# Performance work log

Hardware: AMD Instinct MI355X
Metric: run time of the kernel (lower is better)

Reference implementation:

```python
import jax, jax.numpy as jnp
import numpy as np


def setup_inputs() -> dict:
    key = jax.random.key(0)
    ks = jax.random.split(key, 8)
    B, T, D, H, R = 64, 1024, 512, 512, 64
    s = lambda n: 1.0 / np.sqrt(n)
    return {
        "x":   jax.random.normal(ks[0], (B, T, D), jnp.float32),
        "W_w": jax.random.normal(ks[1], (4 * H, D), jnp.float32) * s(D),
        "W_b": jax.random.normal(ks[2], (4 * H,), jnp.float32) * 0.01,
        "U_w": jax.random.normal(ks[3], (4 * H, H), jnp.float32) * s(H),
        "U_b": jax.random.normal(ks[4], (4 * H,), jnp.float32) * 0.01,
        "A_w": jax.random.normal(ks[5], (R, D), jnp.float32) * s(D),
        "B_w": jax.random.normal(ks[6], (R, H), jnp.float32) * s(H),
        "P_w": jax.random.normal(ks[7], (H, R), jnp.float32) * s(R),
    }


def reference(x, W_w, W_b, U_w, U_b, A_w, B_w, P_w):
    # x: [B,T,D]. Dropout is identity (eval mode).
    Bsz, T, _ = x.shape
    H = U_w.shape[0] // 4
    # Precompute all input-side projections in parallel (no recurrence dep).
    Wx = jnp.einsum('btd,hd->bth', x, W_w) + W_b          # [B,T,4H]
    Ax = jnp.einsum('btd,rd->btr', x, A_w)                # [B,T,R]

    def step(carry, inp):
        h, c = carry
        wx_t, ax_t = inp                                  # [B,4H], [B,R]
        gates = wx_t + h @ U_w.T + U_b                    # [B,4H]
        i, f, o, g = jnp.split(gates, 4, axis=-1)
        i = jax.nn.sigmoid(i)
        f = jax.nn.sigmoid(f)
        o = jax.nn.sigmoid(o)
        g = jnp.tanh(g)
        mix = (ax_t * (h @ B_w.T)) @ P_w.T                # [B,H]
        c = f * c + i * g + 0.1 * mix
        h = o * jnp.tanh(c)
        return (h, c), h

    h0 = jnp.zeros((Bsz, H), x.dtype)
    c0 = jnp.zeros((Bsz, H), x.dtype)
    (h, c), outs = jax.lax.scan(
        step, (h0, c0),
        (jnp.swapaxes(Wx, 0, 1), jnp.swapaxes(Ax, 0, 1)))
    outs = jnp.swapaxes(outs, 0, 1)                       # [B,T,H]
    return outs, h, c
```

## Files before the change

### kernel.cpp

```cpp
#include <hip/hip_runtime.h>
#include <stdint.h>


typedef float    f32x4  __attribute__((ext_vector_type(4)));
typedef __bf16   bf16x8 __attribute__((ext_vector_type(8)));
typedef uint16_t u16;
typedef uint16_t u16x8  __attribute__((ext_vector_type(8)));
typedef uint32_t u32x4  __attribute__((ext_vector_type(4)));

#define WS_XB     0
#define WS_WC     67108864
#define WS_BIAS   69337088
#define WS_U      69345792
#define WS_BW     71442944
#define WS_P      71508480
#define WS_HBUF   71574016
#define WS_MBOX   71705088
#define WS_WXC    71721472

#define OUT_H     33554432
#define OUT_C     33587200

__device__ __forceinline__ u16 f2bf(float f) {
  uint32_t u = __builtin_bit_cast(uint32_t, f);
  u = (u + 0x7fffu + ((u >> 16) & 1u)) >> 16;
  return (u16)u;
}
__device__ __forceinline__ float bf2f(u16 b) {
  uint32_t u = ((uint32_t)b) << 16;
  return __builtin_bit_cast(float, u);
}
__device__ __forceinline__ f32x4 mfma16(u16x8 a, u16x8 b, f32x4 c) {
  return __builtin_amdgcn_mfma_f32_16x16x32_bf16(
      __builtin_bit_cast(bf16x8, a), __builtin_bit_cast(bf16x8, b), c, 0, 0, 0);
}
__device__ __forceinline__ float sigm(float x) { return 1.f / (1.f + __expf(-x)); }
__device__ __forceinline__ float tanh_fast(float x) {
  float a = fabsf(x);
  float e = __expf(2.f * a);
  float t = 1.f - 2.f / (e + 1.f);
  return x < 0.f ? -t : t;
}
__device__ __forceinline__ void lds_barrier() {
  asm volatile("s_waitcnt lgkmcnt(0)" ::: "memory");
  __builtin_amdgcn_sched_barrier(0);
  __builtin_amdgcn_s_barrier();
  __builtin_amdgcn_sched_barrier(0);
}

__global__ void cast_x(const float* __restrict__ x, u16* __restrict__ xb) {
  int i = blockIdx.x * 256 + threadIdx.x;
  const float4* src = (const float4*)x;
  float4 a = src[(size_t)i * 2];
  float4 b = src[(size_t)i * 2 + 1];
  u16x8 o;
  o[0] = f2bf(a.x); o[1] = f2bf(a.y); o[2] = f2bf(a.z); o[3] = f2bf(a.w);
  o[4] = f2bf(b.x); o[5] = f2bf(b.y); o[6] = f2bf(b.z); o[7] = f2bf(b.w);
  *(u16x8*)(xb + (size_t)i * 8) = o;
}

__global__ void prep(const float* __restrict__ W_w, const float* __restrict__ W_b,
                     const float* __restrict__ U_w, const float* __restrict__ U_b,
                     const float* __restrict__ A_w, const float* __restrict__ B_w,
                     const float* __restrict__ P_w,
                     u16* __restrict__ Wc, float* __restrict__ bias,
                     u16* __restrict__ Ubf, u16* __restrict__ Bwbf,
                     u16* __restrict__ Pbf, uint32_t* __restrict__ mbox) {
  const int total = 1114112 + 1048576 + 32768 + 32768 + 2176 + 4096;
  for (int i = blockIdx.x * blockDim.x + threadIdx.x; i < total;
       i += gridDim.x * blockDim.x) {
    int idx = i;
    if (idx < 1114112) {
      int row = idx >> 9, k = idx & 511;
      float v = 0.f;
      if (row < 2048) v = W_w[row * 512 + k];
      else if (row < 2112) v = A_w[(row - 2048) * 512 + k];
      Wc[idx] = f2bf(v);
      continue;
    }
    idx -= 1114112;
    if (idx < 1048576) { Ubf[idx] = f2bf(U_w[idx]); continue; }
    idx -= 1048576;
    if (idx < 32768) { Bwbf[idx] = f2bf(B_w[idx]); continue; }
    idx -= 32768;
    if (idx < 32768) { Pbf[idx] = f2bf(0.1f * P_w[idx]); continue; }
    idx -= 32768;
    if (idx < 2176) {
      bias[idx] = (idx < 2048) ? (W_b[idx] + U_b[idx]) : 0.f;
      continue;
    }
    idx -= 2176;
    mbox[idx] = 0;
  }
}

__global__ void __launch_bounds__(256) gemm_wxc(const u16* __restrict__ xb,
                                                const u16* __restrict__ Wc,
                                                const float* __restrict__ bias,
                                                u16* __restrict__ outWx) {
  __shared__ u16 Atile[128 * 64];
  __shared__ u16 Btile[128 * 64];
  const int n0 = blockIdx.x * 128;
  const int m0 = blockIdx.y * 128;
  const int tid = threadIdx.x, ln = tid & 63, wv = tid >> 6;
  const int wm = (wv >> 1) * 64, wn = (wv & 1) * 64;
  f32x4 acc[4][4] = {};

  for (int k0 = 0; k0 < 512; k0 += 64) {
    __syncthreads();
    #pragma unroll
    for (int q = 0; q < 4; ++q) {
      int idx = tid + q * 256;
      int row = idx >> 3, kc = idx & 7;
      uint4 va = *(const uint4*)(xb + (size_t)(m0 + row) * 512 + k0 + kc * 8);
      *(uint4*)((char*)Atile + row * 128 + ((kc * 16) ^ ((row & 7) << 4))) = va;
      uint4 vb = *(const uint4*)(Wc + (size_t)(n0 + row) * 512 + k0 + kc * 8);
      *(uint4*)((char*)Btile + row * 128 + ((kc * 16) ^ ((row & 7) << 4))) = vb;
    }
    __syncthreads();
    #pragma unroll
    for (int kk = 0; kk < 64; kk += 32) {
      u16x8 af[4], bf[4];
      const int kb = kk * 2 + ((ln >> 4) << 4);
      #pragma unroll
      for (int i = 0; i < 4; ++i) {
        int arow = wm + i * 16 + (ln & 15);
        af[i] = *(const u16x8*)((char*)Atile + arow * 128 + (kb ^ ((arow & 7) << 4)));
        int brow = wn + i * 16 + (ln & 15);
        bf[i] = *(const u16x8*)((char*)Btile + brow * 128 + (kb ^ ((brow & 7) << 4)));
      }
      #pragma unroll
      for (int i = 0; i < 4; ++i)
        #pragma unroll
        for (int j = 0; j < 4; ++j)
          acc[i][j] = mfma16(af[i], bf[j], acc[i][j]);
    }
  }
  #pragma unroll
  for (int i = 0; i < 4; ++i) {
    const int mrow = m0 + wm + i * 16 + ((ln >> 4) << 2);
    #pragma unroll
    for (int j = 0; j < 4; ++j) {
      const int n = n0 + wn + j * 16 + (ln & 15);
      if (n < 2112) {
        const float bv = bias[n];
        #pragma unroll
        for (int r = 0; r < 4; ++r)
          outWx[(size_t)(mrow + r) * 2112 + n] = f2bf(acc[i][j][r] + bv);
      }
    }
  }
}

__global__ void __launch_bounds__(512, 2) recurrent(const u16* __restrict__ Wxc,
                                                    const u16* __restrict__ Ubf,
                                                    const u16* __restrict__ Bwbf,
                                                    const u16* __restrict__ Pbf,
                                                    u16* __restrict__ hbuf,
                                                    uint32_t* __restrict__ mbox,
                                                    float* __restrict__ out) {
  __shared__ char  h_lds[16 * 1024];
  __shared__ float v_buf[16 * 68];
  __shared__ float g_buf[4 * 16 * 17];

  const int tid = threadIdx.x;
  const int wv = tid >> 6, ln = tid & 63;
  const int grp = blockIdx.x & 3;
  const int ublk = blockIdx.x >> 2;
  const int u0 = ublk << 4, b0 = grp << 4;

  uint32_t* mb_grp = mbox + grp * 32 * 32;
  uint32_t* my_line = mb_grp + ublk * 32;

  u16x8 bfrag[16];
  {
    const u16* src = (wv < 4)
        ? (Ubf + (size_t)(wv * 512 + u0 + (ln & 15)) * 512)
        : (Bwbf + (size_t)((wv - 4) * 16 + (ln & 15)) * 512);
    #pragma unroll
    for (int ks = 0; ks < 16; ++ks)
      bfrag[ks] = *(const u16x8*)(src + ks * 32 + ((ln >> 4) << 3));
  }
  u16x8 pfrag[2];
  #pragma unroll
  for (int ks = 0; ks < 2; ++ks)
    pfrag[ks] = *(const u16x8*)(Pbf + (size_t)(u0 + (ln & 15)) * 64 + ks * 32 + ((ln >> 4) << 3));

  for (int i = tid; i < 1024; i += 512)
    ((u32x4*)h_lds)[i] = (u32x4){0u, 0u, 0u, 0u};
  __syncthreads();

  const int arow_base = (ln & 15) * 1024;
  const int a_xor = (ln & 7) << 4;
  const int a_k0 = (ln >> 4) << 4;

  uint32_t wx_cur[4] = {0, 0, 0, 0};
  u16x8 ax0_cur = {}, ax1_cur = {};
  {
    if (wv < 4) {
      const int col = wv * 512 + u0 + (ln & 15);
      const size_t rb = ((size_t)(b0 + ((ln >> 4) << 2)) * 1024 + 0) * 2112;
      #pragma unroll
      for (int j = 0; j < 4; ++j) wx_cur[j] = Wxc[rb + (size_t)j * 1024 * 2112 + col];
    }
    if (wv == 0) {
      const u16* axp = Wxc + ((size_t)(b0 + (ln & 15)) * 1024 + 0) * 2112 + 2048 + ((ln >> 4) << 3);
      ax0_cur = *(const u16x8*)(axp);
      ax1_cur = *(const u16x8*)(axp + 32);
    }
  }

  float c_reg[4] = {0.f, 0.f, 0.f, 0.f};
  float h_last[4] = {0.f, 0.f, 0.f, 0.f};

  #pragma unroll 1
  for (int t = 0; t < 1024; ++t) {
    f32x4 acc0 = {0.f, 0.f, 0.f, 0.f}, acc1 = {0.f, 0.f, 0.f, 0.f};
    #pragma unroll
    for (int ks = 0; ks < 16; ks += 2) {
      u16x8 a0 = *(const u16x8*)(h_lds + arow_base + ((ks * 64 + a_k0) ^ a_xor));
      u16x8 a1 = *(const u16x8*)(h_lds + arow_base + (((ks + 1) * 64 + a_k0) ^ a_xor));
      acc0 = mfma16(a0, bfrag[ks], acc0);
      acc1 = mfma16(a1, bfrag[ks + 1], acc1);
    }
    const f32x4 acc = acc0 + acc1;

    if (wv >= 4) {
      const int r = ((wv - 4) << 4) + (ln & 15);
      const int br = (ln >> 4) << 2;
      #pragma unroll
      for (int j = 0; j < 4; ++j) v_buf[(br + j) * 68 + r] = acc[j];
    } else {
      const int gi = wv * 272 + (ln & 15);
      const int br = (ln >> 4) << 2;
      #pragma unroll
      for (int j = 0; j < 4; ++j) {
        float g = acc[j] + bf2f((u16)wx_cur[j]);
        g = (wv == 3) ? tanh_fast(g) : sigm(g);
        g_buf[gi + (br + j) * 17] = g;
      }
    }
    lds_barrier();

    if (wv == 0) {
      __builtin_amdgcn_s_setprio(1);
      f32x4 accm = {0.f, 0.f, 0.f, 0.f};
      const int bb = ln & 15;
      const int r0 = (ln >> 4) << 3;
      u16x8 af;
      #pragma unroll
      for (int i = 0; i < 8; ++i)
        af[i] = f2bf(bf2f(ax0_cur[i]) * v_buf[bb * 68 + r0 + i]);
      accm = mfma16(af, pfrag[0], accm);
      #pragma unroll
      for (int i = 0; i < 8; ++i)
        af[i] = f2bf(bf2f(ax1_cur[i]) * v_buf[bb * 68 + 32 + r0 + i]);
      accm = mfma16(af, pfrag[1], accm);
      const int u = ln & 15;
      const int brb = (ln >> 4) * 4;
      u16* hdst = hbuf + (size_t)(t & 1) * 32768;
      float hv[4];
      #pragma unroll
      for (int j = 0; j < 4; ++j) {
        const int go = (brb + j) * 17 + u;
        float iv = g_buf[go];
        float fv = g_buf[272 + go];
        float ov = g_buf[544 + go];
        float gv = g_buf[816 + go];
        c_reg[j] = fv * c_reg[j] + iv * gv + accm[j];
        hv[j] = ov * tanh_fast(c_reg[j]);
        h_last[j] = hv[j];
        __hip_atomic_store(hdst + (size_t)(b0 + brb + j) * 512 + u0 + u,
                           f2bf(hv[j]), __ATOMIC_RELAXED, __HIP_MEMORY_SCOPE_AGENT);
      }
      asm volatile("s_waitcnt vmcnt(0)" ::: "memory");
      if (ln < 32)
        __hip_atomic_store(mb_grp + ln * 32 + ublk, (uint32_t)(t + 1),
                           __ATOMIC_RELAXED, __HIP_MEMORY_SCOPE_AGENT);
      __builtin_amdgcn_s_setprio(0);
      #pragma unroll
      for (int j = 0; j < 4; ++j)
        out[((size_t)(b0 + brb + j) * 1024 + t) * 512 + u0 + u] = hv[j];
      {
        const int tn = (t < 1023) ? t + 1 : 1023;
        const u16* axp = Wxc + ((size_t)(b0 + (ln & 15)) * 1024 + tn) * 2112 + 2048 + ((ln >> 4) << 3);
        ax0_cur = *(const u16x8*)(axp);
        ax1_cur = *(const u16x8*)(axp + 32);
        const int col = u0 + (ln & 15);
        const size_t rb = ((size_t)(b0 + ((ln >> 4) << 2)) * 1024 + tn) * 2112;
        #pragma unroll
        for (int j = 0; j < 4; ++j) wx_cur[j] = Wxc[rb + (size_t)j * 1024 * 2112 + col];
      }
    } else if (wv == 1) {
      uint32_t* fp = my_line + (ln & 31);
      const uint32_t target = (uint32_t)(t + 1);
      while (true) {
        uint32_t f = __hip_atomic_load(fp, __ATOMIC_RELAXED, __HIP_MEMORY_SCOPE_AGENT);
        if (__ballot(f >= target) == ~0ull) break;
      }
      const int tn = (t < 1023) ? t + 1 : 1023;
      const int col = 512 + u0 + (ln & 15);
      const size_t rb = ((size_t)(b0 + ((ln >> 4) << 2)) * 1024 + tn) * 2112;
      #pragma unroll
      for (int j = 0; j < 4; ++j) wx_cur[j] = Wxc[rb + (size_t)j * 1024 * 2112 + col];
    } else if (wv < 4) {
      const int tn = (t < 1023) ? t + 1 : 1023;
      const int col = wv * 512 + u0 + (ln & 15);
      const size_t rb = ((size_t)(b0 + ((ln >> 4) << 2)) * 1024 + tn) * 2112;
      #pragma unroll
      for (int j = 0; j < 4; ++j) wx_cur[j] = Wxc[rb + (size_t)j * 1024 * 2112 + col];
    }
    lds_barrier();

    {
      const int row0 = tid >> 6, kc = tid & 63;
      const u16* base = hbuf + (size_t)(t & 1) * 32768 + (size_t)b0 * 512 + kc * 8;
      const u16* p0 = base + (size_t)row0 * 512;
      const u16* p1 = base + (size_t)(row0 + 8) * 512;
      u32x4 v0, v1;
      asm volatile(
          "global_load_dwordx4 %0, %2, off sc1\n\t"
          "global_load_dwordx4 %1, %3, off sc1\n\t"
          "s_waitcnt vmcnt(0)"
          : "=&v"(v0), "=&v"(v1)
          : "v"(p0), "v"(p1)
          : "memory");
      *(u32x4*)(h_lds + row0 * 1024 + ((kc * 16) ^ ((row0 & 7) << 4))) = v0;
      *(u32x4*)(h_lds + (row0 + 8) * 1024 + ((kc * 16) ^ (((row0 + 8) & 7) << 4))) = v1;
    }
    lds_barrier();
  }

  if (wv == 0) {
    const int u = ln & 15, brb = (ln >> 4) * 4;
    #pragma unroll
    for (int j = 0; j < 4; ++j) {
      out[OUT_H + (size_t)(b0 + brb + j) * 512 + u0 + u] = h_last[j];
      out[OUT_C + (size_t)(b0 + brb + j) * 512 + u0 + u] = c_reg[j];
    }
  }
}

extern "C" void kernel_launch(void* const* d_in, const int* in_sizes, int n_in,
                              void* d_out, int out_size, void* d_ws, size_t ws_size,
                              hipStream_t stream) {
  const float* x   = (const float*)d_in[0];
  const float* W_w = (const float*)d_in[1];
  const float* W_b = (const float*)d_in[2];
  const float* U_w = (const float*)d_in[3];
  const float* U_b = (const float*)d_in[4];
  const float* A_w = (const float*)d_in[5];
  const float* B_w = (const float*)d_in[6];
  const float* P_w = (const float*)d_in[7];
  char* ws = (char*)d_ws;

  u16*      xb   = (u16*)(ws + WS_XB);
  u16*      Wc   = (u16*)(ws + WS_WC);
  float*    bias = (float*)(ws + WS_BIAS);
  u16*      Ubf  = (u16*)(ws + WS_U);
  u16*      Bwbf = (u16*)(ws + WS_BW);
  u16*      Pbf  = (u16*)(ws + WS_P);
  u16*      hbuf = (u16*)(ws + WS_HBUF);
  uint32_t* mbox = (uint32_t*)(ws + WS_MBOX);
  u16*      Wxc  = (u16*)(ws + WS_WXC);
  float*    outp = (float*)d_out;

  cast_x<<<16384, 256, 0, stream>>>(x, xb);
  prep<<<2048, 256, 0, stream>>>(W_w, W_b, U_w, U_b, A_w, B_w, P_w,
                                 Wc, bias, Ubf, Bwbf, Pbf, mbox);
  gemm_wxc<<<dim3(17, 512), 256, 0, stream>>>(xb, Wc, bias, Wxc);

  void* args[] = { &Wxc, &Ubf, &Bwbf, &Pbf, &hbuf, &mbox, &outp };
  hipError_t e = hipLaunchCooperativeKernel((const void*)recurrent, dim3(128),
                                            dim3(512), args, 0, stream);
  if (e != hipSuccess) {
    recurrent<<<dim3(128), dim3(512), 0, stream>>>(Wxc, Ubf, Bwbf, Pbf,
                                                   hbuf, mbox, outp);
  }
}
```

Measured before the change: 3.885 ms.

## Interleave two batch groups per block to overlap cross-block h exchange

Each recurrent block now owns two 16-row batch groups instead of one, so the grid drops from 128 to 64 blocks. The gate GEMM for the second group runs while the first group's hidden state is being published and its flags polled. The next-step Wx/Ax prefetch now sits between the two hbuf load batches, and hbuf writes are skipped on the last step. This aims to hide global-memory synchronisation latency behind compute. The cost is twice the serial per-step work on each block and double-buffered LDS.

```diff
diff --git a/kernel.cpp b/kernel.cpp
--- a/kernel.cpp
+++ b/kernel.cpp
@@ -152,6 +152,89 @@
   }
 }
 
+__device__ __forceinline__ void phase1(int wv, int ln, const char* hl,
+                                       float* vb, float* gb,
+                                       const u16x8 (&bfrag)[16],
+                                       const uint32_t (&wx)[4],
+                                       int arow_base, int a_xor, int a_k0) {
+  f32x4 acc0 = {0.f, 0.f, 0.f, 0.f}, acc1 = {0.f, 0.f, 0.f, 0.f};
+  #pragma unroll
+  for (int ks = 0; ks < 16; ks += 2) {
+    u16x8 a0 = *(const u16x8*)(hl + arow_base + ((ks * 64 + a_k0) ^ a_xor));
+    u16x8 a1 = *(const u16x8*)(hl + arow_base + (((ks + 1) * 64 + a_k0) ^ a_xor));
+    acc0 = mfma16(a0, bfrag[ks], acc0);
+    acc1 = mfma16(a1, bfrag[ks + 1], acc1);
+  }
+  const f32x4 acc = acc0 + acc1;
+  if (wv >= 4) {
+    const int r = ((wv - 4) << 4) + (ln & 15);
+    const int br = (ln >> 4) << 2;
+    #pragma unroll
+    for (int j = 0; j < 4; ++j) vb[(br + j) * 68 + r] = acc[j];
+  } else {
+    const int gi = wv * 272 + (ln & 15);
+    const int br = (ln >> 4) << 2;
+    #pragma unroll
+    for (int j = 0; j < 4; ++j) {
+      float gg = acc[j] + bf2f((u16)wx[j]);
+      gg = (wv == 3) ? tanh_fast(gg) : sigm(gg);
+      gb[gi + (br + j) * 17] = gg;
+    }
+  }
+}
+
+__device__ __forceinline__ void produce_step(int t, int ln, int u0, int b0g,
+                                             int cblk, int mgrp,
+                                             const float* vb, const float* gb,
+                                             const u16x8& ax0, const u16x8& ax1,
+                                             const u16x8 (&pfrag)[2],
+                                             u16* hbuf, uint32_t* mbox,
+                                             float* out,
+                                             float (&c_reg)[4], float (&h_last)[4]) {
+  __builtin_amdgcn_s_setprio(1);
+  f32x4 accm = {0.f, 0.f, 0.f, 0.f};
+  const int bb = ln & 15;
+  const int r0 = (ln >> 4) << 3;
+  u16x8 af;
+  #pragma unroll
+  for (int i = 0; i < 8; ++i)
+    af[i] = f2bf(bf2f(ax0[i]) * vb[bb * 68 + r0 + i]);
+  accm = mfma16(af, pfrag[0], accm);
+  #pragma unroll
+  for (int i = 0; i < 8; ++i)
+    af[i] = f2bf(bf2f(ax1[i]) * vb[bb * 68 + 32 + r0 + i]);
+  accm = mfma16(af, pfrag[1], accm);
+  const int u = ln & 15;
+  const int brb = (ln >> 4) * 4;
+  float hv[4];
+  #pragma unroll
+  for (int j = 0; j < 4; ++j) {
+    const int go = (brb + j) * 17 + u;
+    float iv = gb[go];
+    float fv = gb[272 + go];
+    float ov = gb[544 + go];
+    float gv = gb[816 + go];
+    c_reg[j] = fv * c_reg[j] + iv * gv + accm[j];
+    hv[j] = ov * tanh_fast(c_reg[j]);
+    h_last[j] = hv[j];
+  }
+  if (t < 1023) {
+    u16* hdst = hbuf + (size_t)(t & 1) * 32768;
+    #pragma unroll
+    for (int j = 0; j < 4; ++j)
+      __hip_atomic_store(hdst + (size_t)(b0g + brb + j) * 512 + u0 + u,
+                         f2bf(hv[j]), __ATOMIC_RELAXED, __HIP_MEMORY_SCOPE_AGENT);
+    asm volatile("s_waitcnt vmcnt(0)" ::: "memory");
+    if (ln < 32)
+      __hip_atomic_store(mbox + ((size_t)mgrp * 32 + ln) * 32 + cblk,
+                         (uint32_t)(t + 1), __ATOMIC_RELAXED, __HIP_MEMORY_SCOPE_AGENT);
+  }
+  __builtin_amdgcn_s_setprio(0);
+  #pragma unroll
+  for (int j = 0; j < 4; ++j)
+    out[((size_t)(b0g + brb + j) * 1024 + t) * 512 + u0 + u] = hv[j];
+}
+
 __global__ void __launch_bounds__(512, 2) recurrent(const u16* __restrict__ Wxc,
                                                     const u16* __restrict__ Ubf,
                                                     const u16* __restrict__ Bwbf,
@@ -159,18 +242,18 @@
                                                     u16* __restrict__ hbuf,
                                                     uint32_t* __restrict__ mbox,
                                                     float* __restrict__ out) {
-  __shared__ char  h_lds[16 * 1024];
-  __shared__ float v_buf[16 * 68];
-  __shared__ float g_buf[4 * 16 * 17];
+  __shared__ char  h_lds[2][16 * 1024];
+  __shared__ float v_buf[2][16 * 68];
+  __shared__ float g_buf[2][4 * 16 * 17];
 
   const int tid = threadIdx.x;
   const int wv = tid >> 6, ln = tid & 63;
-  const int grp = blockIdx.x & 3;
-  const int ublk = blockIdx.x >> 2;
-  const int u0 = ublk << 4, b0 = grp << 4;
-
-  uint32_t* mb_grp = mbox + grp * 32 * 32;
-  uint32_t* my_line = mb_grp + ublk * 32;
+  const int pair = blockIdx.x >> 5;
+  const int cblk = blockIdx.x & 31;
+  const int u0 = cblk << 4;
+  const int b0g0 = pair << 5;
+  const int b0g1 = b0g0 + 16;
+  const int mg0 = pair * 2, mg1 = mg0 + 1;
 
   u16x8 bfrag[16];
   {
@@ -186,25 +269,30 @@
   for (int ks = 0; ks < 2; ++ks)
     pfrag[ks] = *(const u16x8*)(Pbf + (size_t)(u0 + (ln & 15)) * 64 + ks * 32 + ((ln >> 4) << 3));
 
-  for (int i = tid; i < 1024; i += 512)
+  for (int i = tid; i < 2048; i += 512)
     ((u32x4*)h_lds)[i] = (u32x4){0u, 0u, 0u, 0u};
   __syncthreads();
 
   const int arow_base = (ln & 15) * 1024;
   const int a_xor = (ln & 7) << 4;
   const int a_k0 = (ln >> 4) << 4;
-
-  uint32_t wx_cur[4] = {0, 0, 0, 0};
+  const int ax_b0 = b0g0 + ((wv & 4) << 2);
+
+  uint32_t wx_cur[2][4] = {};
   u16x8 ax0_cur = {}, ax1_cur = {};
   {
     if (wv < 4) {
       const int col = wv * 512 + u0 + (ln & 15);
-      const size_t rb = ((size_t)(b0 + ((ln >> 4) << 2)) * 1024 + 0) * 2112;
       #pragma unroll
-      for (int j = 0; j < 4; ++j) wx_cur[j] = Wxc[rb + (size_t)j * 1024 * 2112 + col];
-    }
-    if (wv == 0) {
-      const u16* axp = Wxc + ((size_t)(b0 + (ln & 15)) * 1024 + 0) * 2112 + 2048 + ((ln >> 4) << 3);
+      for (int g2 = 0; g2 < 2; ++g2) {
+        const size_t rb = ((size_t)(b0g0 + g2 * 16 + ((ln >> 4) << 2)) * 1024 + 0) * 2112;
+        #pragma unroll
+        for (int j = 0; j < 4; ++j)
+          wx_cur[g2][j] = Wxc[rb + (size_t)j * 1024 * 2112 + col];
+      }
+    }
+    if ((wv & 3) == 0) {
+      const u16* axp = Wxc + ((size_t)(ax_b0 + (ln & 15)) * 1024 + 0) * 2112 + 2048 + ((ln >> 4) << 3);
       ax0_cur = *(const u16x8*)(axp);
       ax1_cur = *(const u16x8*)(axp + 32);
     }
@@ -215,128 +303,102 @@
 
   #pragma unroll 1
   for (int t = 0; t < 1024; ++t) {
-    f32x4 acc0 = {0.f, 0.f, 0.f, 0.f}, acc1 = {0.f, 0.f, 0.f, 0.f};
-    #pragma unroll
-    for (int ks = 0; ks < 16; ks += 2) {
-      u16x8 a0 = *(const u16x8*)(h_lds + arow_base + ((ks * 64 + a_k0) ^ a_xor));
-      u16x8 a1 = *(const u16x8*)(h_lds + arow_base + (((ks + 1) * 64 + a_k0) ^ a_xor));
-      acc0 = mfma16(a0, bfrag[ks], acc0);
-      acc1 = mfma16(a1, bfrag[ks + 1], acc1);
-    }
-    const f32x4 acc = acc0 + acc1;
-
-    if (wv >= 4) {
-      const int r = ((wv - 4) << 4) + (ln & 15);
-      const int br = (ln >> 4) << 2;
-      #pragma unroll
-      for (int j = 0; j < 4; ++j) v_buf[(br + j) * 68 + r] = acc[j];
-    } else {
-      const int gi = wv * 272 + (ln & 15);
-      const int br = (ln >> 4) << 2;
-      #pragma unroll
-      for (int j = 0; j < 4; ++j) {
-        float g = acc[j] + bf2f((u16)wx_cur[j]);
-        g = (wv == 3) ? tanh_fast(g) : sigm(g);
-        g_buf[gi + (br + j) * 17] = g;
-      }
-    }
+    phase1(wv, ln, h_lds[0], v_buf[0], g_buf[0], bfrag, wx_cur[0],
+           arow_base, a_xor, a_k0);
     lds_barrier();
-
-    if (wv == 0) {
-      __builtin_amdgcn_s_setprio(1);
-      f32x4 accm = {0.f, 0.f, 0.f, 0.f};
-      const int bb = ln & 15;
-      const int r0 = (ln >> 4) << 3;
-      u16x8 af;
-      #pragma unroll
-      for (int i = 0; i < 8; ++i)
-        af[i] = f2bf(bf2f(ax0_cur[i]) * v_buf[bb * 68 + r0 + i]);
-      accm = mfma16(af, pfrag[0], accm);
-      #pragma unroll
-      for (int i = 0; i < 8; ++i)
-        af[i] = f2bf(bf2f(ax1_cur[i]) * v_buf[bb * 68 + 32 + r0 + i]);
-      accm = mfma16(af, pfrag[1], accm);
-      const int u = ln & 15;
-      const int brb = (ln >> 4) * 4;
-      u16* hdst = hbuf + (size_t)(t & 1) * 32768;
-      float hv[4];
-      #pragma unroll
-      for (int j = 0; j < 4; ++j) {
-        const int go = (brb + j) * 17 + u;
-        float iv = g_buf[go];
-        float fv = g_buf[272 + go];
-        float ov = g_buf[544 + go];
-        float gv = g_buf[816 + go];
-        c_reg[j] = fv * c_reg[j] + iv * gv + accm[j];
-        hv[j] = ov * tanh_fast(c_reg[j]);
-        h_last[j] = hv[j];
-        __hip_atomic_store(hdst + (size_t)(b0 + brb + j) * 512 + u0 + u,
-                           f2bf(hv[j]), __ATOMIC_RELAXED, __HIP_MEMORY_SCOPE_AGENT);
-      }
-      asm volatile("s_waitcnt vmcnt(0)" ::: "memory");
-      if (ln < 32)
-        __hip_atomic_store(mb_grp + ln * 32 + ublk, (uint32_t)(t + 1),
-                           __ATOMIC_RELAXED, __HIP_MEMORY_SCOPE_AGENT);
-      __builtin_amdgcn_s_setprio(0);
-      #pragma unroll
-      for (int j = 0; j < 4; ++j)
-        out[((size_t)(b0 + brb + j) * 1024 + t) * 512 + u0 + u] = hv[j];
-      {
-        const int tn = (t < 1023) ? t + 1 : 1023;
-        const u16* axp = Wxc + ((size_t)(b0 + (ln & 15)) * 1024 + tn) * 2112 + 2048 + ((ln >> 4) << 3);
-        ax0_cur = *(const u16x8*)(axp);
-        ax1_cur = *(const u16x8*)(axp + 32);
-        const int col = u0 + (ln & 15);
-        const size_t rb = ((size_t)(b0 + ((ln >> 4) << 2)) * 1024 + tn) * 2112;
-        #pragma unroll
-        for (int j = 0; j < 4; ++j) wx_cur[j] = Wxc[rb + (size_t)j * 1024 * 2112 + col];
-      }
-    } else if (wv == 1) {
-      uint32_t* fp = my_line + (ln & 31);
+    if (wv == 0)
+      produce_step(t, ln, u0, b0g0, cblk, mg0, v_buf[0], g_buf[0],
+                   ax0_cur, ax1_cur, pfrag, hbuf, mbox, out, c_reg, h_last);
+    phase1(wv, ln, h_lds[1], v_buf[1], g_buf[1], bfrag, wx_cur[1],
+           arow_base, a_xor, a_k0);
+    lds_barrier();
+    if (wv == 4)
+      produce_step(t, ln, u0, b0g1, cblk, mg1, v_buf[1], g_buf[1],
+                   ax0_cur, ax1_cur, pfrag, hbuf, mbox, out, c_reg, h_last);
+    if (wv == 1 && t < 1023) {
+      uint32_t* fp = mbox + ((size_t)mg0 * 32 + cblk) * 32 + (ln & 31);
       const uint32_t target = (uint32_t)(t + 1);
       while (true) {
         uint32_t f = __hip_atomic_load(fp, __ATOMIC_RELAXED, __HIP_MEMORY_SCOPE_AGENT);
         if (__ballot(f >= target) == ~0ull) break;
       }
-      const int tn = (t < 1023) ? t + 1 : 1023;
-      const int col = 512 + u0 + (ln & 15);
-      const size_t rb = ((size_t)(b0 + ((ln >> 4) << 2)) * 1024 + tn) * 2112;
-      #pragma unroll
-      for (int j = 0; j < 4; ++j) wx_cur[j] = Wxc[rb + (size_t)j * 1024 * 2112 + col];
-    } else if (wv < 4) {
-      const int tn = (t < 1023) ? t + 1 : 1023;
-      const int col = wv * 512 + u0 + (ln & 15);
-      const size_t rb = ((size_t)(b0 + ((ln >> 4) << 2)) * 1024 + tn) * 2112;
-      #pragma unroll
-      for (int j = 0; j < 4; ++j) wx_cur[j] = Wxc[rb + (size_t)j * 1024 * 2112 + col];
     }
     lds_barrier();
 
-    {
+    if (t < 1023) {
       const int row0 = tid >> 6, kc = tid & 63;
-      const u16* base = hbuf + (size_t)(t & 1) * 32768 + (size_t)b0 * 512 + kc * 8;
-      const u16* p0 = base + (size_t)row0 * 512;
-      const u16* p1 = base + (size_t)(row0 + 8) * 512;
-      u32x4 v0, v1;
+      const u16* base0 = hbuf + (size_t)(t & 1) * 32768 + (size_t)(b0g0) * 512 + kc * 8;
+      const u16* p0 = base0 + (size_t)row0 * 512;
+      const u16* p1 = base0 + (size_t)(row0 + 8) * 512;
+      u32x4 r0a, r0b;
+      asm volatile(
+          "global_load_dwordx4 %0, %2, off sc1\n\t"
+          "global_load_dwordx4 %1, %3, off sc1"
+          : "=&v"(r0a), "=&v"(r0b) : "v"(p0), "v"(p1) : "memory");
+
+      {
+        const int tn = t + 1;
+        if (wv < 4) {
+          const int col = wv * 512 + u0 + (ln & 15);
+          #pragma unroll
+          for (int g2 = 0; g2 < 2; ++g2) {
+            const size_t rb = ((size_t)(b0g0 + g2 * 16 + ((ln >> 4) << 2)) * 1024 + tn) * 2112;
+            #pragma unroll
+            for (int j = 0; j < 4; ++j)
+              wx_cur[g2][j] = Wxc[rb + (size_t)j * 1024 * 2112 + col];
+          }
+        }
+        if ((wv & 3) == 0) {
+          const u16* axp = Wxc + ((size_t)(ax_b0 + (ln & 15)) * 1024 + tn) * 2112 + 2048 + ((ln >> 4) << 3);
+          ax0_cur = *(const u16x8*)(axp);
+          ax1_cur = *(const u16x8*)(axp + 32);
+        }
+      }
+
+      if (wv == 1) {
+        uint32_t* fp = mbox + ((size_t)mg1 * 32 + cblk) * 32 + (ln & 31);
+        const uint32_t target = (uint32_t)(t + 1);
+        while (true) {
+          uint32_t f = __hip_atomic_load(fp, __ATOMIC_RELAXED, __HIP_MEMORY_SCOPE_AGENT);
+          if (__ballot(f >= target) == ~0ull) break;
+        }
+      }
+      lds_barrier();
+
+      asm volatile("s_waitcnt vmcnt(0)" ::: "memory");
+      __builtin_amdgcn_sched_barrier(0);
+      *(u32x4*)(h_lds[0] + row0 * 1024 + ((kc * 16) ^ ((row0 & 7) << 4))) = r0a;
+      *(u32x4*)(h_lds[0] + (row0 + 8) * 1024 + ((kc * 16) ^ (((row0 + 8) & 7) << 4))) = r0b;
+
+      const u16* base1 = hbuf + (size_t)(t & 1) * 32768 + (size_t)(b0g1) * 512 + kc * 8;
+      const u16* q0 = base1 + (size_t)row0 * 512;
+      const u16* q1 = base1 + (size_t)(row0 + 8) * 512;
+      u32x4 r1a, r1b;
       asm volatile(
           "global_load_dwordx4 %0, %2, off sc1\n\t"
           "global_load_dwordx4 %1, %3, off sc1\n\t"
           "s_waitcnt vmcnt(0)"
-          : "=&v"(v0), "=&v"(v1)
-          : "v"(p0), "v"(p1)
-          : "memory");
-      *(u32x4*)(h_lds + row0 * 1024 + ((kc * 16) ^ ((row0 & 7) << 4))) = v0;
-      *(u32x4*)(h_lds + (row0 + 8) * 1024 + ((kc * 16) ^ (((row0 + 8) & 7) << 4))) = v1;
-    }
-    lds_barrier();
+          : "=&v"(r1a), "=&v"(r1b) : "v"(q0), "v"(q1) : "memory");
+      __builtin_amdgcn_sched_barrier(0);
+      *(u32x4*)(h_lds[1] + row0 * 1024 + ((kc * 16) ^ ((row0 & 7) << 4))) = r1a;
+      *(u32x4*)(h_lds[1] + (row0 + 8) * 1024 + ((kc * 16) ^ (((row0 + 8) & 7) << 4))) = r1b;
+      lds_barrier();
+    }
   }
 
   if (wv == 0) {
     const int u = ln & 15, brb = (ln >> 4) * 4;
     #pragma unroll
     for (int j = 0; j < 4; ++j) {
-      out[OUT_H + (size_t)(b0 + brb + j) * 512 + u0 + u] = h_last[j];
-      out[OUT_C + (size_t)(b0 + brb + j) * 512 + u0 + u] = c_reg[j];
+      out[OUT_H + (size_t)(b0g0 + brb + j) * 512 + u0 + u] = h_last[j];
+      out[OUT_C + (size_t)(b0g0 + brb + j) * 512 + u0 + u] = c_reg[j];
+    }
+  } else if (wv == 4) {
+    const int u = ln & 15, brb = (ln >> 4) * 4;
+    #pragma unroll
+    for (int j = 0; j < 4; ++j) {
+      out[OUT_H + (size_t)(b0g1 + brb + j) * 512 + u0 + u] = h_last[j];
+      out[OUT_C + (size_t)(b0g1 + brb + j) * 512 + u0 + u] = c_reg[j];
     }
   }
 }
@@ -371,10 +433,10 @@
   gemm_wxc<<<dim3(17, 512), 256, 0, stream>>>(xb, Wc, bias, Wxc);
 
   void* args[] = { &Wxc, &Ubf, &Bwbf, &Pbf, &hbuf, &mbox, &outp };
-  hipError_t e = hipLaunchCooperativeKernel((const void*)recurrent, dim3(128),
+  hipError_t e = hipLaunchCooperativeKernel((const void*)recurrent, dim3(64),
                                             dim3(512), args, 0, stream);
   if (e != hipSuccess) {
-    recurrent<<<dim3(128), dim3(512), 0, stream>>>(Wxc, Ubf, Bwbf, Pbf,
-                                                   hbuf, mbox, outp);
-  }
-}
+    recurrent<<<dim3(64), dim3(512), 0, stream>>>(Wxc, Ubf, Bwbf, Pbf,
+                                                  hbuf, mbox, outp);
+  }
+}
```

New measurement: 5.396 ms. 1.39x slower.

## Publish h tiles via LDS-staged wide stores and poll mailbox across three waves

Applied to the files above, without the earlier changes.

Each block now stages its 16x16 bf16 h tile in LDS and publishes it with a few 16-byte stores into a tile-major hbuf layout, replacing per-element 2-byte atomic stores. The consumer side reads the tile-major layout with wide loads and scatters 8-byte pieces into swizzled LDS. Mailbox polling moves from wave 1 alone to waves 1-3, which share an LDS flag so any of them can end the wait early. Next-step Wx/Ax prefetches move after the barrier, and the last step skips publishing. The aim is to cut per-step cross-block communication latency on the serial recurrence, at the cost of an extra LDS round-trip and more polling traffic.

```diff
diff --git a/kernel.cpp b/kernel.cpp
--- a/kernel.cpp
+++ b/kernel.cpp
@@ -6,6 +6,7 @@
 typedef __bf16   bf16x8 __attribute__((ext_vector_type(8)));
 typedef uint16_t u16;
 typedef uint16_t u16x8  __attribute__((ext_vector_type(8)));
+typedef uint32_t u32x2  __attribute__((ext_vector_type(2)));
 typedef uint32_t u32x4  __attribute__((ext_vector_type(4)));
 
 #define WS_XB     0
@@ -162,6 +163,8 @@
   __shared__ char  h_lds[16 * 1024];
   __shared__ float v_buf[16 * 68];
   __shared__ float g_buf[4 * 16 * 17];
+  __shared__ u16   hpub[16 * 16];
+  __shared__ int   poll_done;
 
   const int tid = threadIdx.x;
   const int wv = tid >> 6, ln = tid & 63;
@@ -170,7 +173,6 @@
   const int u0 = ublk << 4, b0 = grp << 4;
 
   uint32_t* mb_grp = mbox + grp * 32 * 32;
-  uint32_t* my_line = mb_grp + ublk * 32;
 
   u16x8 bfrag[16];
   {
@@ -188,11 +190,13 @@
 
   for (int i = tid; i < 1024; i += 512)
     ((u32x4*)h_lds)[i] = (u32x4){0u, 0u, 0u, 0u};
+  if (tid == 0) poll_done = 0;
   __syncthreads();
 
   const int arow_base = (ln & 15) * 1024;
   const int a_xor = (ln & 7) << 4;
   const int a_k0 = (ln >> 4) << 4;
+  const int r_blk = tid >> 4, r_b = tid & 15;
 
   uint32_t wx_cur[4] = {0, 0, 0, 0};
   u16x8 ax0_cur = {}, ax1_cur = {};
@@ -258,7 +262,6 @@
       accm = mfma16(af, pfrag[1], accm);
       const int u = ln & 15;
       const int brb = (ln >> 4) * 4;
-      u16* hdst = hbuf + (size_t)(t & 1) * 32768;
       float hv[4];
       #pragma unroll
       for (int j = 0; j < 4; ++j) {
@@ -270,63 +273,78 @@
         c_reg[j] = fv * c_reg[j] + iv * gv + accm[j];
         hv[j] = ov * tanh_fast(c_reg[j]);
         h_last[j] = hv[j];
-        __hip_atomic_store(hdst + (size_t)(b0 + brb + j) * 512 + u0 + u,
-                           f2bf(hv[j]), __ATOMIC_RELAXED, __HIP_MEMORY_SCOPE_AGENT);
-      }
-      asm volatile("s_waitcnt vmcnt(0)" ::: "memory");
-      if (ln < 32)
-        __hip_atomic_store(mb_grp + ln * 32 + ublk, (uint32_t)(t + 1),
-                           __ATOMIC_RELAXED, __HIP_MEMORY_SCOPE_AGENT);
+      }
+      if (t < 1023) {
+        #pragma unroll
+        for (int j = 0; j < 4; ++j)
+          hpub[(brb + j) * 16 + u] = f2bf(hv[j]);
+        asm volatile("s_waitcnt lgkmcnt(0)" ::: "memory");
+        __builtin_amdgcn_sched_barrier(0);
+        if (ln < 32) {
+          u32x4 pv = *(const u32x4*)((const char*)hpub + ln * 16);
+          u16* dst = hbuf + ((size_t)(((t & 1) * 4 + grp) * 32 + ublk)) * 256 + ln * 8;
+          asm volatile("global_store_dwordx4 %0, %1, off sc1"
+                       :: "v"(dst), "v"(pv) : "memory");
+        }
+        asm volatile("s_waitcnt vmcnt(0)" ::: "memory");
+        if (ln < 32)
+          __hip_atomic_store(mb_grp + ln * 32 + ublk, (uint32_t)(t + 1),
+                             __ATOMIC_RELAXED, __HIP_MEMORY_SCOPE_AGENT);
+      }
       __builtin_amdgcn_s_setprio(0);
       #pragma unroll
       for (int j = 0; j < 4; ++j)
         out[((size_t)(b0 + brb + j) * 1024 + t) * 512 + u0 + u] = hv[j];
+    }
+
+    if (wv >= 1 && wv <= 3 && t < 1023) {
+      volatile int* dsf = &poll_done;
+      uint32_t* fp = mb_grp + ublk * 32 + (ln & 31);
+      const int target = t + 1;
+      while (true) {
+        if (*dsf >= target) break;
+        uint32_t f = __hip_atomic_load(fp, __ATOMIC_RELAXED, __HIP_MEMORY_SCOPE_AGENT);
+        if (__ballot((int)f >= target) == ~0ull) {
+          if (ln == 0) *dsf = target;
+          break;
+        }
+      }
+    }
+    lds_barrier();
+
+    if (t < 1023) {
+      const u16* src = hbuf + ((size_t)(((t & 1) * 4 + grp) * 32 + r_blk)) * 256 + r_b * 16;
+      u32x4 A, B;
+      asm volatile(
+          "global_load_dwordx4 %0, %2, off sc1\n\t"
+          "global_load_dwordx4 %1, %2, off offset:16 sc1\n\t"
+          "s_waitcnt vmcnt(0)"
+          : "=&v"(A), "=&v"(B) : "v"(src) : "memory");
+      __builtin_amdgcn_sched_barrier(0);
       {
-        const int tn = (t < 1023) ? t + 1 : 1023;
-        const u16* axp = Wxc + ((size_t)(b0 + (ln & 15)) * 1024 + tn) * 2112 + 2048 + ((ln >> 4) << 3);
+        const int base = r_blk * 32;
+        const int xorb = (r_b & 7) << 4;
+        u32x2 w;
+        w[0] = A[0]; w[1] = A[1];
+        *(u32x2*)(h_lds + r_b * 1024 + ((base + 0) ^ xorb)) = w;
+        w[0] = A[2]; w[1] = A[3];
+        *(u32x2*)(h_lds + r_b * 1024 + ((base + 8) ^ xorb)) = w;
+        w[0] = B[0]; w[1] = B[1];
+        *(u32x2*)(h_lds + r_b * 1024 + ((base + 16) ^ xorb)) = w;
+        w[0] = B[2]; w[1] = B[3];
+        *(u32x2*)(h_lds + r_b * 1024 + ((base + 24) ^ xorb)) = w;
+      }
+      if (wv < 4) {
+        const int col = wv * 512 + u0 + (ln & 15);
+        const size_t rb = ((size_t)(b0 + ((ln >> 4) << 2)) * 1024 + t + 1) * 2112;
+        #pragma unroll
+        for (int j = 0; j < 4; ++j) wx_cur[j] = Wxc[rb + (size_t)j * 1024 * 2112 + col];
+      }
+      if (wv == 0) {
+        const u16* axp = Wxc + ((size_t)(b0 + (ln & 15)) * 1024 + t + 1) * 2112 + 2048 + ((ln >> 4) << 3);
         ax0_cur = *(const u16x8*)(axp);
         ax1_cur = *(const u16x8*)(axp + 32);
-        const int col = u0 + (ln & 15);
-        const size_t rb = ((size_t)(b0 + ((ln >> 4) << 2)) * 1024 + tn) * 2112;
-        #pragma unroll
-        for (int j = 0; j < 4; ++j) wx_cur[j] = Wxc[rb + (size_t)j * 1024 * 2112 + col];
-      }
-    } else if (wv == 1) {
-      uint32_t* fp = my_line + (ln & 31);
-      const uint32_t target = (uint32_t)(t + 1);
-      while (true) {
-        uint32_t f = __hip_atomic_load(fp, __ATOMIC_RELAXED, __HIP_MEMORY_SCOPE_AGENT);
-        if (__ballot(f >= target) == ~0ull) break;
-      }
-      const int tn = (t < 1023) ? t + 1 : 1023;
-      const int col = 512 + u0 + (ln & 15);
-      const size_t rb = ((size_t)(b0 + ((ln >> 4) << 2)) * 1024 + tn) * 2112;
-      #pragma unroll
-      for (int j = 0; j < 4; ++j) wx_cur[j] = Wxc[rb + (size_t)j * 1024 * 2112 + col];
-    } else if (wv < 4) {
-      const int tn = (t < 1023) ? t + 1 : 1023;
-      const int col = wv * 512 + u0 + (ln & 15);
-      const size_t rb = ((size_t)(b0 + ((ln >> 4) << 2)) * 1024 + tn) * 2112;
-      #pragma unroll
-      for (int j = 0; j < 4; ++j) wx_cur[j] = Wxc[rb + (size_t)j * 1024 * 2112 + col];
-    }
-    lds_barrier();
-
-    {
-      const int row0 = tid >> 6, kc = tid & 63;
-      const u16* base = hbuf + (size_t)(t & 1) * 32768 + (size_t)b0 * 512 + kc * 8;
-      const u16* p0 = base + (size_t)row0 * 512;
-      const u16* p1 = base + (size_t)(row0 + 8) * 512;
-      u32x4 v0, v1;
-      asm volatile(
-          "global_load_dwordx4 %0, %2, off sc1\n\t"
-          "global_load_dwordx4 %1, %3, off sc1\n\t"
-          "s_waitcnt vmcnt(0)"
-          : "=&v"(v0), "=&v"(v1)
-          : "v"(p0), "v"(p1)
-          : "memory");
-      *(u32x4*)(h_lds + row0 * 1024 + ((kc * 16) ^ ((row0 & 7) << 4))) = v0;
-      *(u32x4*)(h_lds + (row0 + 8) * 1024 + ((kc * 16) ^ (((row0 + 8) & 7) << 4))) = v1;
+      }
     }
     lds_barrier();
   }
```

New measurement: 4.176 ms. 1.08x slower.
